# Kernel optimization log

Measured on AMD Instinct MI355X. Metric: run time of the kernel, lower is better.

Reference implementation:

```python
import jax, jax.numpy as jnp
import numpy as np

NEG_SLOPE = 0.2  # PyG GATConv default negative_slope
N_NODES = 100000


def gat_conv(x, W, a_src, a_dst, src, dst, n_nodes):
    """One PyG-style GATConv (eval mode, self-loops already in src/dst).
    x: [N, in], W: [in, H*O], a_src/a_dst: [H, O]. Returns [N, H, O]."""
    heads, out_ch = a_src.shape
    h = (x @ W).reshape(n_nodes, heads, out_ch)          # [N,H,O]
    al_src = jnp.einsum('nho,ho->nh', h, a_src)          # [N,H]
    al_dst = jnp.einsum('nho,ho->nh', h, a_dst)          # [N,H]
    e = jax.nn.leaky_relu(al_src[src] + al_dst[dst], NEG_SLOPE)  # [E,H]
    # segment softmax over incoming edges of each dst node
    m = jax.ops.segment_max(e, dst, num_segments=n_nodes)       # [N,H]
    e = jnp.exp(e - m[dst])
    denom = jax.ops.segment_sum(e, dst, num_segments=n_nodes)   # [N,H]
    alpha = e / denom[dst]                                       # [E,H]
    msg = h[src] * alpha[:, :, None]                             # [E,H,O]
    return jax.ops.segment_sum(msg, dst, num_segments=n_nodes)  # [N,H,O]


def setup_inputs() -> dict:
    key = jax.random.key(0)
    ks = jax.random.split(key, 10)
    N, E = N_NODES, 3200000
    node_attr_dim, state_dim, heads, out_dim = 128, 8, 8, 1
    hid = state_dim * heads  # 64

    def glorot(k, shape, fan_in, fan_out):
        return jax.random.normal(k, shape, dtype=jnp.float32) * np.sqrt(2.0 / (fan_in + fan_out)).astype(np.float32)

    x = jax.random.normal(ks[0], (N, node_attr_dim), dtype=jnp.float32)
    edge_index = jax.random.randint(ks[1], (2, E), 0, N, dtype=jnp.int64)
    W1 = glorot(ks[2], (node_attr_dim, heads * state_dim), node_attr_dim, heads * state_dim)
    a_src1 = glorot(ks[3], (heads, state_dim), state_dim, 1)
    a_dst1 = glorot(ks[4], (heads, state_dim), state_dim, 1)
    b1 = jnp.zeros((hid,), dtype=jnp.float32)
    W2 = glorot(ks[5], (hid, out_dim), hid, out_dim)
    a_src2 = glorot(ks[6], (1, out_dim), out_dim, 1)
    a_dst2 = glorot(ks[7], (1, out_dim), out_dim, 1)
    b2 = jnp.zeros((out_dim,), dtype=jnp.float32)
    return {"x": x, "W1": W1, "a_src1": a_src1, "a_dst1": a_dst1, "b1": b1,
            "W2": W2, "a_src2": a_src2, "a_dst2": a_dst2, "b2": b2,
            "edge_index": edge_index}


def reference(x, W1, a_src1, a_dst1, b1, W2, a_src2, a_dst2, b2, edge_index):
    n = N_NODES
    loops = jnp.arange(n, dtype=edge_index.dtype)
    src = jnp.concatenate([edge_index[0], loops])  # add self-loops (PyG default)
    dst = jnp.concatenate([edge_index[1], loops])
    # layer 1: heads=8, concat -> [N, 64]
    h1 = gat_conv(x, W1, a_src1, a_dst1, src, dst, n)
    h1 = h1.reshape(n, -1) + b1
    h1 = jax.nn.relu(h1)  # dropout skipped (eval)
    # layer 2: heads=1, concat(size 1) -> [N, 1]
    h2 = gat_conv(h1, W2, a_src2, a_dst2, src, dst, n)
    out = h2.reshape(n, -1) + b2
    return out
```

## Files before the change

kernel.cpp:

```cpp
#include <hip/hip_runtime.h>
#include <math.h>

#define NEG 0.2f
#define CHUNK 16384

__device__ __forceinline__ float lrelu(float v) { return fmaxf(v, NEG * v); }

__device__ __forceinline__ unsigned short f2bf(float f) {
    unsigned u = __float_as_uint(f);
    u = (u + 0x7fffu + ((u >> 16) & 1u)) >> 16;
    return (unsigned short)u;
}

__global__ __launch_bounds__(256) void k1(const float* __restrict__ x,
        const float* __restrict__ W1, const float* __restrict__ a_src,
        const float* __restrict__ a_dst,
        unsigned short* __restrict__ h1b, float* __restrict__ als,
        float* __restrict__ ald, int N)
{
    __shared__ float Wl[128 * 64];
    __shared__ float xt[128][68];

    const int tid = threadIdx.x;
    const int base = blockIdx.x * 64;

    const float4* Wv = (const float4*)W1;
    float4* Wlv = (float4*)Wl;
    for (int i = tid; i < 128 * 16; i += 256) Wlv[i] = Wv[i];

    for (int idx = tid; idx < 64 * 32; idx += 256) {
        int nl = idx >> 5;
        int k4 = (idx & 31) * 4;
        int n = base + nl;
        float4 v = make_float4(0.f, 0.f, 0.f, 0.f);
        if (n < N) v = *(const float4*)&x[(size_t)n * 128 + k4];
        xt[k4 + 0][nl] = v.x;
        xt[k4 + 1][nl] = v.y;
        xt[k4 + 2][nl] = v.z;
        xt[k4 + 3][nl] = v.w;
    }
    __syncthreads();

    const int wave = tid >> 6, lane = tid & 63;
    const int g = lane >> 4, c = lane & 15;
    const int nl0 = wave * 16 + 4 * g;

    float acc[4][4];
    #pragma unroll
    for (int j = 0; j < 4; ++j)
        #pragma unroll
        for (int t = 0; t < 4; ++t) acc[j][t] = 0.f;

    #pragma unroll 4
    for (int k = 0; k < 128; ++k) {
        float4 wv = *(const float4*)&Wl[k * 64 + 4 * c];
        float4 xv = *(const float4*)&xt[k][nl0];
        const float xs[4] = {xv.x, xv.y, xv.z, xv.w};
        const float wsv[4] = {wv.x, wv.y, wv.z, wv.w};
        #pragma unroll
        for (int j = 0; j < 4; ++j)
            #pragma unroll
            for (int t = 0; t < 4; ++t)
                acc[j][t] = fmaf(xs[j], wsv[t], acc[j][t]);
    }

    float a_s[4], a_d[4];
    #pragma unroll
    for (int t = 0; t < 4; ++t) { a_s[t] = a_src[4 * c + t]; a_d[t] = a_dst[4 * c + t]; }

    #pragma unroll
    for (int j = 0; j < 4; ++j) {
        int n = base + nl0 + j;
        float ps = 0.f, pd = 0.f;
        #pragma unroll
        for (int t = 0; t < 4; ++t) {
            ps = fmaf(acc[j][t], a_s[t], ps);
            pd = fmaf(acc[j][t], a_d[t], pd);
        }
        ps += __shfl_xor(ps, 1, 64);
        pd += __shfl_xor(pd, 1, 64);
        if (n < N) {
            ushort4 hb;
            hb.x = f2bf(acc[j][0]); hb.y = f2bf(acc[j][1]);
            hb.z = f2bf(acc[j][2]); hb.w = f2bf(acc[j][3]);
            *(ushort4*)&h1b[(size_t)n * 64 + 4 * c] = hb;
            if ((c & 1) == 0) {
                als[n * 8 + (c >> 1)] = ps;
                ald[n * 8 + (c >> 1)] = pd;
            }
        }
    }
}


__global__ __launch_bounds__(256) void p1(const int* __restrict__ ei, int E, int N,
        int* __restrict__ T, int NB, int NC)
{
    extern __shared__ int hist[];
    int tid = threadIdx.x;
    for (int b = tid; b < NB; b += 256) hist[b] = 0;
    __syncthreads();
    int base = blockIdx.x * CHUNK;
    for (int i = tid; i < CHUNK; i += 256) {
        int e = base + i;
        if (e >= E) break;
        int d = ei[E + e];
        if ((unsigned)d < (unsigned)N) atomicAdd(&hist[d >> 8], 1);
    }
    __syncthreads();
    for (int b = tid; b < NB; b += 256) T[b * NC + blockIdx.x] = hist[b];
}

__global__ __launch_bounds__(256) void p2a(int* __restrict__ T,
        int* __restrict__ total, int NB, int NC)
{
    int wave = threadIdx.x >> 6, lane = threadIdx.x & 63;
    int b = blockIdx.x * 4 + wave;
    if (b >= NB) return;
    int run = 0;
    for (int j0 = 0; j0 < NC; j0 += 64) {
        int j = j0 + lane;
        int orig = (j < NC) ? T[b * NC + j] : 0;
        int v = orig;
        #pragma unroll
        for (int off = 1; off < 64; off <<= 1) {
            int t = __shfl_up(v, off, 64);
            if (lane >= off) v += t;
        }
        if (j < NC) T[b * NC + j] = run + v - orig;
        run += __shfl(v, 63, 64);
    }
    if (lane == 0) total[b] = run;
}

__global__ __launch_bounds__(512) void p2b(const int* __restrict__ total,
        int* __restrict__ bstart, int nb)
{
    __shared__ int s[512];
    int tid = threadIdx.x;
    int run = 0;
    for (int base = 0; base < nb; base += 512) {
        int i = base + tid;
        int orig = (i < nb) ? total[i] : 0;
        s[tid] = orig;
        __syncthreads();
        #pragma unroll
        for (int off = 1; off < 512; off <<= 1) {
            int t = (tid >= off) ? s[tid - off] : 0;
            __syncthreads();
            s[tid] += t;
            __syncthreads();
        }
        if (i < nb) bstart[i] = run + s[tid] - orig;
        int tot = s[511];
        __syncthreads();
        run += tot;
    }
    if (tid == 0) bstart[nb] = run;
}

__global__ __launch_bounds__(256) void p3(const int* __restrict__ ei, int E, int N,
        const int* __restrict__ T, const int* __restrict__ bstart,
        unsigned* __restrict__ tmp, int NB, int NC)
{
    extern __shared__ int cur[];
    int tid = threadIdx.x;
    int j = blockIdx.x;
    for (int b = tid; b < NB; b += 256) cur[b] = bstart[b] + T[b * NC + j];
    __syncthreads();
    int base = j * CHUNK;
    for (int i = tid; i < CHUNK; i += 256) {
        int e = base + i;
        if (e >= E) break;
        int d = ei[E + e];
        if ((unsigned)d >= (unsigned)N) continue;
        int s = ei[e];
        if ((unsigned)s >= (unsigned)N) s = 0;
        int pos = atomicAdd(&cur[d >> 8], 1);
        if ((unsigned)pos < (unsigned)E)
            tmp[pos] = (unsigned)s | ((unsigned)(d & 255) << 24);
    }
}

__global__ __launch_bounds__(256) void p4(const unsigned* __restrict__ tmp,
        const int* __restrict__ bstart,
        int* __restrict__ cnt, int* __restrict__ rowptr, int* __restrict__ csr,
        int N, int E)
{
    __shared__ int hist[256];
    __shared__ int ssc[256];
    __shared__ int cur[256];
    int tid = threadIdx.x;
    int b = blockIdx.x;
    int s0 = bstart[b], s1 = bstart[b + 1];
    if (s0 < 0) s0 = 0; if (s0 > E) s0 = E;
    if (s1 < s0) s1 = s0; if (s1 > E) s1 = E;

    hist[tid] = 0;
    __syncthreads();
    for (int i = s0 + tid; i < s1; i += 256)
        atomicAdd(&hist[tmp[i] >> 24], 1);
    __syncthreads();

    int h = hist[tid];
    ssc[tid] = h;
    __syncthreads();
    #pragma unroll
    for (int off = 1; off < 256; off <<= 1) {
        int t = (tid >= off) ? ssc[tid - off] : 0;
        __syncthreads();
        ssc[tid] += t;
        __syncthreads();
    }
    int excl = ssc[tid] - h;
    int node = b * 256 + tid;
    if (node < N) {
        cnt[node] = h;
        rowptr[node] = s0 + excl;
    }
    cur[tid] = s0 + excl;
    __syncthreads();

    for (int i = s0 + tid; i < s1; i += 256) {
        unsigned v = tmp[i];
        int pos = atomicAdd(&cur[v >> 24], 1);
        if ((unsigned)pos < (unsigned)E) csr[pos] = (int)(v & 0xFFFFFFu);
    }
}


__global__ __launch_bounds__(256) void kh(const int* __restrict__ ei, int E, int N,
                                          int* __restrict__ cnt)
{
    int e = blockIdx.x * 256 + threadIdx.x;
    if (e >= E) return;
    int d = ei[E + e];
    if ((unsigned)d < (unsigned)N) atomicAdd(&cnt[d], 1);
}

__global__ __launch_bounds__(256) void ka(const int* __restrict__ cnt,
        int* __restrict__ rowptr, int* __restrict__ cursor,
        int* __restrict__ gtotal, int N)
{
    __shared__ int s[256];
    __shared__ int base;
    int tid = threadIdx.x;
    int g = blockIdx.x * 256 + tid;
    int v = (g < N) ? cnt[g] : 0;
    s[tid] = v;
    __syncthreads();
    #pragma unroll
    for (int off = 1; off < 256; off <<= 1) {
        int t = (tid >= off) ? s[tid - off] : 0;
        __syncthreads();
        s[tid] += t;
        __syncthreads();
    }
    if (tid == 255) base = atomicAdd(gtotal, s[255]);
    __syncthreads();
    if (g < N) {
        int r = base + s[tid] - v;
        rowptr[g] = r;
        cursor[g] = r;
    }
}

__global__ __launch_bounds__(256) void kc(const int* __restrict__ ei, int E, int N,
        int* __restrict__ cursor, int* __restrict__ csr)
{
    int e = blockIdx.x * 256 + threadIdx.x;
    if (e >= E) return;
    int s = ei[e];
    int d = ei[E + e];
    if ((unsigned)d >= (unsigned)N) return;
    int p = atomicAdd(&cursor[d], 1);
    if ((unsigned)p < (unsigned)E) csr[p] = s;
}

__global__ __launch_bounds__(256) void g1(const int* __restrict__ csr,
        const int* __restrict__ rowptr, const int* __restrict__ cnt,
        const unsigned short* __restrict__ h1b, const float* __restrict__ als,
        const float* __restrict__ ald,
        const float* __restrict__ b1, const float* __restrict__ W2,
        const float* __restrict__ a_src2, const float* __restrict__ a_dst2,
        float2* __restrict__ h2a, float* __restrict__ ald2, int N, int E)
{
    __shared__ float wl[4][8 * 65];
    __shared__ int   sl[4][64];
    __shared__ int   csh[4];

    const int wave = threadIdx.x >> 6, lane = threadIdx.x & 63;
    const int n = blockIdx.x * 4 + wave;
    const bool active = (n < N);
    const int n2 = active ? n : 0;

    const int s = lane >> 5;
    const int cp = lane & 31;
    const int hp = cp >> 2;

    const unsigned* h1w = (const unsigned*)h1b;
    const float4* als4 = (const float4*)als;
    const float4* ald4 = (const float4*)ald;

    float4 d0 = ald4[n2 * 2], d1 = ald4[n2 * 2 + 1];
    float aldv[8] = {d0.x, d0.y, d0.z, d0.w, d1.x, d1.y, d1.z, d1.w};

    float denv[8];
    #pragma unroll
    for (int i = 0; i < 8; ++i) denv[i] = 0.f;
    float acc0 = 0.f, acc1 = 0.f;

    int start = active ? rowptr[n2] : 0;
    int c = active ? cnt[n2] : 0;
    if ((unsigned)start >= (unsigned)E) { start = 0; c = 0; }
    if (c < 0) c = 0;
    if (start + c > E) c = E - start;

    if (lane == 0) csh[wave] = c;
    __syncthreads();
    int cmax = max(max(csh[0], csh[1]), max(csh[2], csh[3]));

    float* wlw = wl[wave];
    int* slw = sl[wave];

    for (int cbase = 0; cbase < cmax; cbase += 64) {
        int rem = c - cbase;
        if (rem > 64) rem = 64;
        if (rem < 0) rem = 0;

        int esrc = 0;
        if (lane < rem) {
            int t = csr[start + cbase + lane];
            if ((unsigned)t < (unsigned)N) esrc = t;
        }
        float4 a0 = als4[esrc * 2], a1 = als4[esrc * 2 + 1];
        float wv[8];
        wv[0] = __expf(lrelu(a0.x + aldv[0]));
        wv[1] = __expf(lrelu(a0.y + aldv[1]));
        wv[2] = __expf(lrelu(a0.z + aldv[2]));
        wv[3] = __expf(lrelu(a0.w + aldv[3]));
        wv[4] = __expf(lrelu(a1.x + aldv[4]));
        wv[5] = __expf(lrelu(a1.y + aldv[5]));
        wv[6] = __expf(lrelu(a1.z + aldv[6]));
        wv[7] = __expf(lrelu(a1.w + aldv[7]));
        if (lane >= rem) {
            #pragma unroll
            for (int i = 0; i < 8; ++i) wv[i] = 0.f;
        }
        #pragma unroll
        for (int i = 0; i < 8; ++i) {
            denv[i] += wv[i];
            wlw[i * 65 + lane] = wv[i];
        }
        slw[lane] = esrc << 5;
        __syncthreads();

        int steps = (rem + 1) >> 1;
        #pragma unroll 4
        for (int i = 0; i < steps; ++i) {
            int ge = 2 * i + s;
            float w = wlw[hp * 65 + ge];
            int soff = slw[ge];
            unsigned u = h1w[soff + cp];
            acc0 = fmaf(w, __uint_as_float(u << 16), acc0);
            acc1 = fmaf(w, __uint_as_float(u & 0xffff0000u), acc1);
        }
        __syncthreads();
    }

    #pragma unroll
    for (int off = 1; off < 64; off <<= 1) {
        #pragma unroll
        for (int i = 0; i < 8; ++i) denv[i] += __shfl_xor(denv[i], off, 64);
    }
    float q0 = (hp & 1) ? denv[1] : denv[0];
    float q1 = (hp & 1) ? denv[3] : denv[2];
    float q2 = (hp & 1) ? denv[5] : denv[4];
    float q3 = (hp & 1) ? denv[7] : denv[6];
    float r0 = (hp & 2) ? q1 : q0;
    float r1 = (hp & 2) ? q3 : q2;
    float den = (hp & 4) ? r1 : r0;

    acc0 += __shfl_xor(acc0, 32, 64);
    acc1 += __shfl_xor(acc1, 32, 64);

    float wsf = __expf(lrelu(als[n2 * 8 + hp] + aldv[hp]));
    unsigned un = h1w[(n2 << 5) + cp];
    den += wsf;
    acc0 = fmaf(wsf, __uint_as_float(un << 16), acc0);
    acc1 = fmaf(wsf, __uint_as_float(un & 0xffff0000u), acc1);

    float2 bb = *(const float2*)&b1[2 * cp];
    float2 w2 = *(const float2*)&W2[2 * cp];
    float v0 = fmaxf(acc0 / den + bb.x, 0.f);
    float v1 = fmaxf(acc1 / den + bb.y, 0.f);
    float t = fmaf(v0, w2.x, v1 * w2.y);
    #pragma unroll
    for (int off = 1; off < 32; off <<= 1) t += __shfl_xor(t, off, 64);
    if (active && lane == 0) {
        float2 p;
        p.x = t;
        p.y = t * a_src2[0];
        h2a[n] = p;
        ald2[n] = t * a_dst2[0];
    }
}

__global__ __launch_bounds__(256) void g2(const int* __restrict__ csr,
        const int* __restrict__ rowptr, const int* __restrict__ cnt,
        const float2* __restrict__ h2a, const float* __restrict__ ald2,
        const float* __restrict__ b2, float* __restrict__ out, int N, int E)
{
    int sub = threadIdx.x >> 5;
    int l32 = threadIdx.x & 31;
    int n = blockIdx.x * 8 + sub;
    if (n >= N) return;

    float ad = ald2[n];
    int start = rowptr[n];
    int c = cnt[n];
    if ((unsigned)start >= (unsigned)E) { start = 0; c = 0; }
    if (c < 0) c = 0;
    if (start + c > E) c = E - start;

    float den = 0.f, acc = 0.f;
    for (int i = l32; i < c; i += 32) {
        int src = csr[start + i];
        if ((unsigned)src >= (unsigned)N) src = 0;
        float2 p = h2a[src];
        float w = __expf(lrelu(p.y + ad));
        den += w;
        acc = fmaf(w, p.x, acc);
    }
    #pragma unroll
    for (int off = 1; off < 32; off <<= 1) {
        den += __shfl_xor(den, off, 32);
        acc += __shfl_xor(acc, off, 32);
    }
    if (l32 == 0) {
        float2 p = h2a[n];
        float w0 = __expf(lrelu(p.y + ad));
        out[n] = (acc + w0 * p.x) / (den + w0) + b2[0];
    }
}

extern "C" void kernel_launch(void* const* d_in, const int* in_sizes, int n_in,
                              void* d_out, int out_size, void* d_ws, size_t ws_size,
                              hipStream_t stream)
{
    const float* x   = (const float*)d_in[0];
    const float* W1  = (const float*)d_in[1];
    const float* as1 = (const float*)d_in[2];
    const float* ad1 = (const float*)d_in[3];
    const float* b1  = (const float*)d_in[4];
    const float* W2  = (const float*)d_in[5];
    const float* as2 = (const float*)d_in[6];
    const float* ad2 = (const float*)d_in[7];
    const float* b2  = (const float*)d_in[8];
    const int*   ei  = (const int*)d_in[9];

    int N = in_sizes[0] / 128;
    int E = in_sizes[9] / 2;
    int NB = (N + 255) >> 8;
    int NC = (E + CHUNK - 1) / CHUNK;

    char* wsb = (char*)d_ws;
    size_t off = 0;
    auto alloc = [&](size_t bytes) -> char* {
        char* p = wsb + off;
        off = (off + bytes + 255) & ~(size_t)255;
        return p;
    };

    unsigned short* h1b = (unsigned short*)alloc((size_t)N * 64 * 2);
    float* als    = (float*)alloc((size_t)N * 8 * 4);
    float* ald    = (float*)alloc((size_t)N * 8 * 4);
    float2* h2a   = (float2*)alloc((size_t)N * 8);
    float* ald2   = (float*)alloc((size_t)N * 4);
    int* cnt      = (int*)alloc((size_t)N * 4);
    int* rowptr   = (int*)alloc((size_t)N * 4);
    int* csr      = (int*)alloc((size_t)E * 4);
    size_t common = off;

    int* T        = (int*)alloc((size_t)NB * NC * 4);
    int* total    = (int*)alloc((size_t)NB * 4);
    int* bstart   = (int*)alloc((size_t)(NB + 1) * 4);
    unsigned* tmp = (unsigned*)alloc((size_t)E * 4);
    size_t need_new = off;

    k1<<<(N + 63) / 64, 256, 0, stream>>>(x, W1, as1, ad1, h1b, als, ald, N);

    if (ws_size >= need_new && NB <= 512) {
        size_t lds = (size_t)NB * 4;
        p1<<<NC, 256, lds, stream>>>(ei, E, N, T, NB, NC);
        p2a<<<(NB + 3) / 4, 256, 0, stream>>>(T, total, NB, NC);
        p2b<<<1, 512, 0, stream>>>(total, bstart, NB);
        p3<<<NC, 256, lds, stream>>>(ei, E, N, T, bstart, tmp, NB, NC);
        p4<<<NB, 256, 0, stream>>>(tmp, bstart, cnt, rowptr, csr, N, E);
    } else {
        off = common;
        int* gtotal = (int*)alloc(32);
        int* cursor = (int*)alloc((size_t)N * 4);
        hipMemsetAsync(cnt, 0, (size_t)N * sizeof(int), stream);
        hipMemsetAsync(gtotal, 0, 32, stream);
        kh<<<(E + 255) / 256, 256, 0, stream>>>(ei, E, N, cnt);
        ka<<<(N + 255) / 256, 256, 0, stream>>>(cnt, rowptr, cursor, gtotal, N);
        kc<<<(E + 255) / 256, 256, 0, stream>>>(ei, E, N, cursor, csr);
    }

    g1<<<(N + 3) / 4, 256, 0, stream>>>(csr, rowptr, cnt, h1b, als, ald,
                                        b1, W2, as2, ad2, h2a, ald2, N, E);
    g2<<<(N + 7) / 8, 256, 0, stream>>>(csr, rowptr, cnt, h2a, ald2, b2,
                                        (float*)d_out, N, E);
}
```

Before: 387.3 us.

## Process two nodes per wave in layer-1 aggregation and store source logits as bf16

The layer-1 gather kernel now assigns two destination nodes per wave, with each half-wave loading 32 edges of its own node. Both halves then cooperatively accumulate features for both nodes. The block-wide barriers are removed. Per-edge source attention logits are stored in bf16 instead of fp32, halving the gather traffic for them. This targets idle lanes for low-degree nodes and memory traffic, at the cost of reduced logit precision and reliance on wave-synchronous LDS access without barriers.

```diff
diff --git a/kernel.cpp b/kernel.cpp
--- a/kernel.cpp
+++ b/kernel.cpp
@@ -11,11 +11,14 @@
     u = (u + 0x7fffu + ((u >> 16) & 1u)) >> 16;
     return (unsigned short)u;
 }
+__device__ __forceinline__ float bf2f(unsigned short s) {
+    return __uint_as_float((unsigned)s << 16);
+}
 
 __global__ __launch_bounds__(256) void k1(const float* __restrict__ x,
         const float* __restrict__ W1, const float* __restrict__ a_src,
         const float* __restrict__ a_dst,
-        unsigned short* __restrict__ h1b, float* __restrict__ als,
+        unsigned short* __restrict__ h1b, unsigned short* __restrict__ als_b,
         float* __restrict__ ald, int N)
 {
     __shared__ float Wl[128 * 64];
@@ -85,7 +88,7 @@
             hb.z = f2bf(acc[j][2]); hb.w = f2bf(acc[j][3]);
             *(ushort4*)&h1b[(size_t)n * 64 + 4 * c] = hb;
             if ((c & 1) == 0) {
-                als[n * 8 + (c >> 1)] = ps;
+                als_b[n * 8 + (c >> 1)] = f2bf(ps);
                 ald[n * 8 + (c >> 1)] = pd;
             }
         }
@@ -279,97 +282,123 @@
 
 __global__ __launch_bounds__(256) void g1(const int* __restrict__ csr,
         const int* __restrict__ rowptr, const int* __restrict__ cnt,
-        const unsigned short* __restrict__ h1b, const float* __restrict__ als,
+        const unsigned short* __restrict__ h1b, const unsigned short* __restrict__ als_b,
         const float* __restrict__ ald,
         const float* __restrict__ b1, const float* __restrict__ W2,
         const float* __restrict__ a_src2, const float* __restrict__ a_dst2,
         float2* __restrict__ h2a, float* __restrict__ ald2, int N, int E)
 {
-    __shared__ float wl[4][8 * 65];
-    __shared__ int   sl[4][64];
-    __shared__ int   csh[4];
+    __shared__ float wl[4][2][8 * 33];
+    __shared__ int   sl[4][2][32];
 
     const int wave = threadIdx.x >> 6, lane = threadIdx.x & 63;
-    const int n = blockIdx.x * 4 + wave;
-    const bool active = (n < N);
-    const int n2 = active ? n : 0;
-
-    const int s = lane >> 5;
+    const int half = lane >> 5;
+    const int slot = lane & 31;
     const int cp = lane & 31;
     const int hp = cp >> 2;
+    const int s = half;
+
+    const int nA = blockIdx.x * 8 + wave * 2;
+    const int nB = nA + 1;
+    const bool actA = (nA < N), actB = (nB < N);
+    const int nA2 = actA ? nA : 0;
+    const int nB2 = actB ? nB : 0;
+    const int nOwn = half ? nB2 : nA2;
 
     const unsigned* h1w = (const unsigned*)h1b;
-    const float4* als4 = (const float4*)als;
     const float4* ald4 = (const float4*)ald;
 
-    float4 d0 = ald4[n2 * 2], d1 = ald4[n2 * 2 + 1];
+    float4 d0 = ald4[nOwn * 2], d1 = ald4[nOwn * 2 + 1];
     float aldv[8] = {d0.x, d0.y, d0.z, d0.w, d1.x, d1.y, d1.z, d1.w};
 
+    int startA = actA ? rowptr[nA2] : 0;
+    int cA = actA ? cnt[nA2] : 0;
+    if ((unsigned)startA >= (unsigned)E) { startA = 0; cA = 0; }
+    if (cA < 0) cA = 0;
+    if (startA + cA > E) cA = E - startA;
+
+    int startB = actB ? rowptr[nB2] : 0;
+    int cB = actB ? cnt[nB2] : 0;
+    if ((unsigned)startB >= (unsigned)E) { startB = 0; cB = 0; }
+    if (cB < 0) cB = 0;
+    if (startB + cB > E) cB = E - startB;
+
+    const int startOwn = half ? startB : startA;
+    const int cOwn = half ? cB : cA;
+    const int cmaxW = max(cA, cB);
+
     float denv[8];
     #pragma unroll
     for (int i = 0; i < 8; ++i) denv[i] = 0.f;
-    float acc0 = 0.f, acc1 = 0.f;
-
-    int start = active ? rowptr[n2] : 0;
-    int c = active ? cnt[n2] : 0;
-    if ((unsigned)start >= (unsigned)E) { start = 0; c = 0; }
-    if (c < 0) c = 0;
-    if (start + c > E) c = E - start;
-
-    if (lane == 0) csh[wave] = c;
-    __syncthreads();
-    int cmax = max(max(csh[0], csh[1]), max(csh[2], csh[3]));
-
-    float* wlw = wl[wave];
-    int* slw = sl[wave];
-
-    for (int cbase = 0; cbase < cmax; cbase += 64) {
-        int rem = c - cbase;
-        if (rem > 64) rem = 64;
-        if (rem < 0) rem = 0;
-
+    float a0A = 0.f, a1A = 0.f, a0B = 0.f, a1B = 0.f;
+
+    float* wlwA = wl[wave][0];
+    float* wlwB = wl[wave][1];
+    float* wlwOwn = half ? wlwB : wlwA;
+    int* slwA = sl[wave][0];
+    int* slwB = sl[wave][1];
+    int* slwOwn = half ? slwB : slwA;
+
+    for (int cbase = 0; cbase < cmaxW; cbase += 32) {
+        int remOwn = cOwn - cbase;
+        if (remOwn > 32) remOwn = 32;
+        if (remOwn < 0) remOwn = 0;
         int esrc = 0;
-        if (lane < rem) {
-            int t = csr[start + cbase + lane];
+        if (slot < remOwn) {
+            int t = csr[startOwn + cbase + slot];
             if ((unsigned)t < (unsigned)N) esrc = t;
         }
-        float4 a0 = als4[esrc * 2], a1 = als4[esrc * 2 + 1];
+        uint4 ub = *(const uint4*)&als_b[esrc * 8];
         float wv[8];
-        wv[0] = __expf(lrelu(a0.x + aldv[0]));
-        wv[1] = __expf(lrelu(a0.y + aldv[1]));
-        wv[2] = __expf(lrelu(a0.z + aldv[2]));
-        wv[3] = __expf(lrelu(a0.w + aldv[3]));
-        wv[4] = __expf(lrelu(a1.x + aldv[4]));
-        wv[5] = __expf(lrelu(a1.y + aldv[5]));
-        wv[6] = __expf(lrelu(a1.z + aldv[6]));
-        wv[7] = __expf(lrelu(a1.w + aldv[7]));
-        if (lane >= rem) {
+        wv[0] = __expf(lrelu(__uint_as_float(ub.x << 16)        + aldv[0]));
+        wv[1] = __expf(lrelu(__uint_as_float(ub.x & 0xffff0000u) + aldv[1]));
+        wv[2] = __expf(lrelu(__uint_as_float(ub.y << 16)        + aldv[2]));
+        wv[3] = __expf(lrelu(__uint_as_float(ub.y & 0xffff0000u) + aldv[3]));
+        wv[4] = __expf(lrelu(__uint_as_float(ub.z << 16)        + aldv[4]));
+        wv[5] = __expf(lrelu(__uint_as_float(ub.z & 0xffff0000u) + aldv[5]));
+        wv[6] = __expf(lrelu(__uint_as_float(ub.w << 16)        + aldv[6]));
+        wv[7] = __expf(lrelu(__uint_as_float(ub.w & 0xffff0000u) + aldv[7]));
+        if (slot >= remOwn) {
             #pragma unroll
             for (int i = 0; i < 8; ++i) wv[i] = 0.f;
         }
         #pragma unroll
         for (int i = 0; i < 8; ++i) {
             denv[i] += wv[i];
-            wlw[i * 65 + lane] = wv[i];
-        }
-        slw[lane] = esrc << 5;
-        __syncthreads();
-
-        int steps = (rem + 1) >> 1;
+            wlwOwn[i * 33 + slot] = wv[i];
+        }
+        slwOwn[slot] = esrc << 5;
+
+        int remA = cA - cbase;
+        if (remA > 32) remA = 32;
+        if (remA < 0) remA = 0;
+        int stepsA = (remA + 1) >> 1;
         #pragma unroll 4
-        for (int i = 0; i < steps; ++i) {
+        for (int i = 0; i < stepsA; ++i) {
             int ge = 2 * i + s;
-            float w = wlw[hp * 65 + ge];
-            int soff = slw[ge];
+            float w = wlwA[hp * 33 + ge];
+            int soff = slwA[ge];
             unsigned u = h1w[soff + cp];
-            acc0 = fmaf(w, __uint_as_float(u << 16), acc0);
-            acc1 = fmaf(w, __uint_as_float(u & 0xffff0000u), acc1);
-        }
-        __syncthreads();
-    }
-
-    #pragma unroll
-    for (int off = 1; off < 64; off <<= 1) {
+            a0A = fmaf(w, __uint_as_float(u << 16), a0A);
+            a1A = fmaf(w, __uint_as_float(u & 0xffff0000u), a1A);
+        }
+        int remB = cB - cbase;
+        if (remB > 32) remB = 32;
+        if (remB < 0) remB = 0;
+        int stepsB = (remB + 1) >> 1;
+        #pragma unroll 4
+        for (int i = 0; i < stepsB; ++i) {
+            int ge = 2 * i + s;
+            float w = wlwB[hp * 33 + ge];
+            int soff = slwB[ge];
+            unsigned u = h1w[soff + cp];
+            a0B = fmaf(w, __uint_as_float(u << 16), a0B);
+            a1B = fmaf(w, __uint_as_float(u & 0xffff0000u), a1B);
+        }
+    }
+
+    #pragma unroll
+    for (int off = 1; off < 32; off <<= 1) {
         #pragma unroll
         for (int i = 0; i < 8; ++i) denv[i] += __shfl_xor(denv[i], off, 64);
     }
@@ -379,30 +408,53 @@
     float q3 = (hp & 1) ? denv[7] : denv[6];
     float r0 = (hp & 2) ? q1 : q0;
     float r1 = (hp & 2) ? q3 : q2;
-    float den = (hp & 4) ? r1 : r0;
-
-    acc0 += __shfl_xor(acc0, 32, 64);
-    acc1 += __shfl_xor(acc1, 32, 64);
-
-    float wsf = __expf(lrelu(als[n2 * 8 + hp] + aldv[hp]));
-    unsigned un = h1w[(n2 << 5) + cp];
-    den += wsf;
-    acc0 = fmaf(wsf, __uint_as_float(un << 16), acc0);
-    acc1 = fmaf(wsf, __uint_as_float(un & 0xffff0000u), acc1);
+    float den_own = (hp & 4) ? r1 : r0;
+    float den_oth = __shfl_xor(den_own, 32, 64);
+    float denA = half ? den_oth : den_own;
+    float denB = half ? den_own : den_oth;
+
+    a0A += __shfl_xor(a0A, 32, 64);
+    a1A += __shfl_xor(a1A, 32, 64);
+    a0B += __shfl_xor(a0B, 32, 64);
+    a1B += __shfl_xor(a1B, 32, 64);
+
+    float wsfA = __expf(lrelu(bf2f(als_b[nA2 * 8 + hp]) + ald[nA2 * 8 + hp]));
+    float wsfB = __expf(lrelu(bf2f(als_b[nB2 * 8 + hp]) + ald[nB2 * 8 + hp]));
+    unsigned uA = h1w[(nA2 << 5) + cp];
+    unsigned uB = h1w[(nB2 << 5) + cp];
+    denA += wsfA;
+    denB += wsfB;
+    a0A = fmaf(wsfA, __uint_as_float(uA << 16), a0A);
+    a1A = fmaf(wsfA, __uint_as_float(uA & 0xffff0000u), a1A);
+    a0B = fmaf(wsfB, __uint_as_float(uB << 16), a0B);
+    a1B = fmaf(wsfB, __uint_as_float(uB & 0xffff0000u), a1B);
 
     float2 bb = *(const float2*)&b1[2 * cp];
     float2 w2 = *(const float2*)&W2[2 * cp];
-    float v0 = fmaxf(acc0 / den + bb.x, 0.f);
-    float v1 = fmaxf(acc1 / den + bb.y, 0.f);
-    float t = fmaf(v0, w2.x, v1 * w2.y);
-    #pragma unroll
-    for (int off = 1; off < 32; off <<= 1) t += __shfl_xor(t, off, 64);
-    if (active && lane == 0) {
-        float2 p;
-        p.x = t;
-        p.y = t * a_src2[0];
-        h2a[n] = p;
-        ald2[n] = t * a_dst2[0];
+    float as2 = a_src2[0], ad2v = a_dst2[0];
+
+    float vA0 = fmaxf(a0A / denA + bb.x, 0.f);
+    float vA1 = fmaxf(a1A / denA + bb.y, 0.f);
+    float tA = fmaf(vA0, w2.x, vA1 * w2.y);
+    float vB0 = fmaxf(a0B / denB + bb.x, 0.f);
+    float vB1 = fmaxf(a1B / denB + bb.y, 0.f);
+    float tB = fmaf(vB0, w2.x, vB1 * w2.y);
+    #pragma unroll
+    for (int off = 1; off < 32; off <<= 1) {
+        tA += __shfl_xor(tA, off, 64);
+        tB += __shfl_xor(tB, off, 64);
+    }
+    if (lane == 0) {
+        if (actA) {
+            float2 p; p.x = tA; p.y = tA * as2;
+            h2a[nA] = p;
+            ald2[nA] = tA * ad2v;
+        }
+        if (actB) {
+            float2 p; p.x = tB; p.y = tB * as2;
+            h2a[nB] = p;
+            ald2[nB] = tB * ad2v;
+        }
     }
 }
 
@@ -472,8 +524,8 @@
         return p;
     };
 
-    unsigned short* h1b = (unsigned short*)alloc((size_t)N * 64 * 2);
-    float* als    = (float*)alloc((size_t)N * 8 * 4);
+    unsigned short* h1b  = (unsigned short*)alloc((size_t)N * 64 * 2);
+    unsigned short* alsb = (unsigned short*)alloc((size_t)N * 8 * 2);
     float* ald    = (float*)alloc((size_t)N * 8 * 4);
     float2* h2a   = (float2*)alloc((size_t)N * 8);
     float* ald2   = (float*)alloc((size_t)N * 4);
@@ -488,7 +540,7 @@
     unsigned* tmp = (unsigned*)alloc((size_t)E * 4);
     size_t need_new = off;
 
-    k1<<<(N + 63) / 64, 256, 0, stream>>>(x, W1, as1, ad1, h1b, als, ald, N);
+    k1<<<(N + 63) / 64, 256, 0, stream>>>(x, W1, as1, ad1, h1b, alsb, ald, N);
 
     if (ws_size >= need_new && NB <= 512) {
         size_t lds = (size_t)NB * 4;
@@ -508,7 +560,7 @@
         kc<<<(E + 255) / 256, 256, 0, stream>>>(ei, E, N, cursor, csr);
     }
 
-    g1<<<(N + 3) / 4, 256, 0, stream>>>(csr, rowptr, cnt, h1b, als, ald,
+    g1<<<(N + 7) / 8, 256, 0, stream>>>(csr, rowptr, cnt, h1b, alsb, ald,
                                         b1, W2, as2, ad2, h2a, ald2, N, E);
     g2<<<(N + 7) / 8, 256, 0, stream>>>(csr, rowptr, cnt, h2a, ald2, b2,
                                         (float*)d_out, N, E);
```

Result: slower. 408.9 us (+5.6%).
